# Performance work log

Measured on AMD Instinct MI355X. Metric: run time of the kernel, lower is better.

## Reference

```python
import jax, jax.numpy as jnp
import numpy as np

B, S, H = 2, 2048, 1024
NH = 16
HD = H // NH  # 64


def _linear_params(key, fan_in, fan_out):
    k1, k2 = jax.random.split(key)
    bound = 1.0 / np.sqrt(fan_in)
    W = jax.random.uniform(k1, (fan_in, fan_out), jnp.float32, -bound, bound)
    b = jax.random.uniform(k2, (fan_out,), jnp.float32, -bound, bound)
    return W, b


def setup_inputs() -> dict:
    key = jax.random.key(0)
    ks = jax.random.split(key, 7)
    hidden_states = jax.random.normal(ks[0], (B, S, H), jnp.float32)
    governance_embeddings = jax.random.normal(ks[1], (B, H), jnp.float32)
    Wq, bq = _linear_params(ks[2], H, H)
    Wk, bk = _linear_params(ks[3], H, H)
    Wv, bv = _linear_params(ks[4], H, H)
    Wgq, bgq = _linear_params(ks[5], H, H)
    Wgk, bgk = _linear_params(ks[6], H, H)
    return {
        'hidden_states': hidden_states,
        'governance_embeddings': governance_embeddings,
        'Wq': Wq, 'bq': bq, 'Wk': Wk, 'bk': bk, 'Wv': Wv, 'bv': bv,
        'Wgq': Wgq, 'bgq': bgq, 'Wgk': Wgk, 'bgk': bgk,
    }


def reference(hidden_states, governance_embeddings, Wq, bq, Wk, bk, Wv, bv, Wgq, bgq, Wgk, bgk):
    b, s, h = hidden_states.shape
    # QKV projections -> [b, nh, s, hd]
    def heads(x):
        return x.reshape(b, s, NH, HD).transpose(0, 2, 1, 3)
    q = heads(hidden_states @ Wq + bq)
    k = heads(hidden_states @ Wk + bk)
    v = heads(hidden_states @ Wv + bv)

    scale = jnp.float32(1.0 / np.sqrt(HD))
    scores = jnp.einsum('bhid,bhjd->bhij', q, k) * scale  # [b,nh,s,s]

    # governance bias: one query per example vs per-token keys (unscaled)
    gq = (governance_embeddings @ Wgq + bgq).reshape(b, NH, HD)      # [b,nh,hd]
    gk = (hidden_states @ Wgk + bgk).reshape(b, s, NH, HD)           # [b,s,nh,hd]
    gov_scores = jnp.einsum('bhd,bshd->bhs', gq, gk)                 # [b,nh,s]

    # bias is constant along key dim (torch expand on last axis)
    combined = scores + 0.1 * gov_scores[..., :, None]

    probs = jax.nn.softmax(combined, axis=-1)  # dropout = identity (eval)
    context = jnp.einsum('bhij,bhjd->bhid', probs, v)
    context = context.transpose(0, 2, 1, 3).reshape(b, s, h)

    entropy = -jnp.sum(probs * jnp.log(probs + 1e-8), axis=-1).mean()
    influence = jnp.abs(gov_scores).mean()  # mean over expanded tensor == mean over [b,nh,s]
    concentration = probs.max(axis=-1).mean()
    return context, entropy, influence, concentration
```

## Files before the change

### kernel.cpp

```cpp
#include <hip/hip_runtime.h>


typedef unsigned short u16;
typedef __attribute__((ext_vector_type(8))) short bf16x8;
typedef __attribute__((ext_vector_type(4))) float f32x4;
typedef __attribute__((ext_vector_type(16))) float f32x16;
typedef __attribute__((ext_vector_type(2))) float f32x2;
typedef __attribute__((ext_vector_type(4))) u16 u16x4;
typedef __attribute__((ext_vector_type(4))) float float4v;

typedef const __attribute__((address_space(1))) void gvoid_t;
typedef __attribute__((address_space(3))) void lvoid_t;

__device__ __forceinline__ void gl_lds16(const void* g, void* l) {
  __builtin_amdgcn_global_load_lds((gvoid_t*)g, (lvoid_t*)l, 16, 0, 0);
}

__device__ __forceinline__ u16 f2bf(float x) {
  union { float f; unsigned u; } v; v.f = x;
  unsigned r = v.u + 0x7fffu + ((v.u >> 16) & 1u);
  return (u16)(r >> 16);
}
__device__ __forceinline__ unsigned pk2(float hi, float lo) {
  union { float f; unsigned u; } a, b; a.f = hi; b.f = lo;
  return __builtin_amdgcn_perm(a.u, b.u, 0x07060302u);
}
__device__ __forceinline__ bf16x8 mk8(unsigned a, unsigned b, unsigned c, unsigned d) {
  union { unsigned u[4]; bf16x8 v; } x;
  x.u[0] = a; x.u[1] = b; x.u[2] = c; x.u[3] = d; return x.v;
}

#if defined(__has_builtin)
#if __has_builtin(__builtin_amdgcn_exp2f)
#define EXP2(x) __builtin_amdgcn_exp2f(x)
#endif
#endif
#ifndef EXP2
#define EXP2(x) exp2f(x)
#endif

__global__ void prep(const float* __restrict__ hs,
                     const float* __restrict__ W0, const float* __restrict__ W1,
                     const float* __restrict__ W2, const float* __restrict__ W3,
                     const float* __restrict__ ge, const float* __restrict__ Wgq,
                     u16* __restrict__ hsB, u16* __restrict__ WB,
                     float* __restrict__ gq_part, float* __restrict__ acc3) {
  __shared__ __align__(16) u16 T[64][72];
  int bx = blockIdx.x, tid = threadIdx.x;
  if (bx < 2048) {
    int i = bx * 256 + tid;
    const float4v* in4 = (const float4v*)hs;
    float4v a = in4[i * 2], b = in4[i * 2 + 1];
    bf16x8 v;
    v[0] = (short)f2bf(a.x); v[1] = (short)f2bf(a.y);
    v[2] = (short)f2bf(a.z); v[3] = (short)f2bf(a.w);
    v[4] = (short)f2bf(b.x); v[5] = (short)f2bf(b.y);
    v[6] = (short)f2bf(b.z); v[7] = (short)f2bf(b.w);
    *(bf16x8*)&hsB[(size_t)i * 8] = v;
    return;
  }
  if (bx < 3072) {
    int idx = bx - 2048;
    int mat = idx >> 8, sub = idx & 255;
    const float* W = (mat == 0) ? W0 : (mat == 1) ? W1 : (mat == 2) ? W2 : W3;
    int k0 = (sub >> 4) * 64, n0 = (sub & 15) * 64;
#pragma unroll
    for (int p = 0; p < 4; ++p) {
      int chunk = p * 256 + tid;
      int row = chunk >> 4, cp = chunk & 15;
      float4v v = *(const float4v*)&W[(size_t)(k0 + row) * 1024 + n0 + cp * 4];
      u16x4 o; o.x = f2bf(v.x); o.y = f2bf(v.y); o.z = f2bf(v.z); o.w = f2bf(v.w);
      *(u16x4*)&T[row][cp * 4] = o;
    }
    __syncthreads();
#pragma unroll
    for (int p = 0; p < 2; ++p) {
      int chunk = p * 256 + tid;
      int nrow = chunk >> 3, cp = chunk & 7;
      bf16x8 v;
#pragma unroll
      for (int e = 0; e < 8; ++e) v[e] = (short)T[cp * 8 + e][nrow];
      *(bf16x8*)&WB[(size_t)(mat * 1024 + n0 + nrow) * 1024 + k0 + cp * 8] = v;
    }
    return;
  }
  {
    int idx = bx - 3072;
    if (idx == 0 && tid < 3) acc3[tid] = 0.f;
    int kb = idx >> 1, b = idx & 1;
    int col0 = tid * 4;
    float4v s = {0.f, 0.f, 0.f, 0.f};
    for (int k = kb * 32; k < kb * 32 + 32; ++k) {
      float g = ge[b * 1024 + k];
      float4v w = *(const float4v*)&Wgq[(size_t)k * 1024 + col0];
      s.x += g * w.x; s.y += g * w.y; s.z += g * w.z; s.w += g * w.w;
    }
    *(float4v*)&gq_part[(size_t)idx * 1024 + col0] = s;
  }
}

__global__ __launch_bounds__(256, 3) void gemm_qkvg(
    const u16* __restrict__ A, const u16* __restrict__ Bw,
    const float* __restrict__ bq, const float* __restrict__ bk,
    const float* __restrict__ bv, const float* __restrict__ bgk,
    const float* __restrict__ bgq, const float* __restrict__ gq_part,
    u16* __restrict__ Qb, u16* __restrict__ Kt4, u16* __restrict__ Vt4,
    float* __restrict__ acc3) {
  __shared__ __align__(16) u16 As[2][128 * 32];
  __shared__ __align__(16) u16 Bs[2][128 * 32];
  __shared__ float redI[4];
  const int tid = threadIdx.x, lane = tid & 63, wv = tid >> 6;
  const int li = lane & 15, quad = lane >> 4;
  const int bid = blockIdx.x;
  const int nb = bid & 31, mb = bid >> 5;
  const u16* Ap = A + (size_t)(mb * 128) * 1024;
  const u16* Bp = Bw + (size_t)(nb * 128) * 1024;
  const int wm0 = (wv >> 1) * 64, wn0 = (wv & 1) * 64;

  f32x4 acc[4][4];
#pragma unroll
  for (int t = 0; t < 4; ++t)
#pragma unroll
    for (int u = 0; u < 4; ++u) acc[t][u] = (f32x4){0.f, 0.f, 0.f, 0.f};

#pragma unroll
  for (int jj = 0; jj < 2; ++jj) {
    int j = wv * 2 + jj;
    int row = j * 16 + (lane >> 2);
    int co = lane & 3;
    gl_lds16(Ap + (size_t)row * 1024 + co * 8, &As[0][j * 512]);
    gl_lds16(Bp + (size_t)row * 1024 + co * 8, &Bs[0][j * 512]);
  }

  for (int kt = 0; kt < 32; ++kt) {
    const int cur = kt & 1;
    __syncthreads();
    if (kt < 31) {
#pragma unroll
      for (int jj = 0; jj < 2; ++jj) {
        int j = wv * 2 + jj;
        int row = j * 16 + (lane >> 2);
        int co = lane & 3;
        gl_lds16(Ap + (size_t)row * 1024 + (kt + 1) * 32 + co * 8, &As[cur ^ 1][j * 512]);
        gl_lds16(Bp + (size_t)row * 1024 + (kt + 1) * 32 + co * 8, &Bs[cur ^ 1][j * 512]);
      }
    }
    bf16x8 af[4], bf[4];
#pragma unroll
    for (int t = 0; t < 4; ++t)
      af[t] = *(const bf16x8*)&As[cur][(wm0 + t * 16 + li) * 32 + quad * 8];
#pragma unroll
    for (int u = 0; u < 4; ++u)
      bf[u] = *(const bf16x8*)&Bs[cur][(wn0 + u * 16 + li) * 32 + quad * 8];
#pragma unroll
    for (int t = 0; t < 4; ++t)
#pragma unroll
      for (int u = 0; u < 4; ++u)
        acc[t][u] = __builtin_amdgcn_mfma_f32_16x16x32_bf16(af[t], bf[u], acc[t][u], 0, 0, 0);
  }

  const int nbase = nb * 128;
  const int mat = nbase >> 10;
  if (mat == 3) {
    const int colbase = nbase & 1023;
    const int bat = (mb * 128) >> 11;
    float gqv[4], bgkv[4];
#pragma unroll
    for (int u2 = 0; u2 < 4; ++u2) {
      int col = colbase + wn0 + u2 * 16 + li;
      float g = bgq[col];
      for (int kb = 0; kb < 32; ++kb)
        g += gq_part[(size_t)(kb * 2 + bat) * 1024 + col];
      gqv[u2] = g;
      bgkv[u2] = bgk[col];
    }
    float infl = 0.f;
#pragma unroll
    for (int t = 0; t < 4; ++t)
#pragma unroll
      for (int r = 0; r < 4; ++r) {
        float v = (acc[t][0][r] + bgkv[0]) * gqv[0];
        v = __builtin_fmaf(acc[t][1][r] + bgkv[1], gqv[1], v);
        v = __builtin_fmaf(acc[t][2][r] + bgkv[2], gqv[2], v);
        v = __builtin_fmaf(acc[t][3][r] + bgkv[3], gqv[3], v);
        v += __shfl_xor(v, 1, 64); v += __shfl_xor(v, 2, 64);
        v += __shfl_xor(v, 4, 64); v += __shfl_xor(v, 8, 64);
        infl += fabsf(v);
      }
    infl = (li == 0) ? infl : 0.f;
    infl += __shfl_xor(infl, 16, 64);
    infl += __shfl_xor(infl, 32, 64);
    if (lane == 0) redI[wv] = infl;
    __syncthreads();
    if (tid == 0) atomicAdd(&acc3[2], redI[0] + redI[1] + redI[2] + redI[3]);
  } else if (mat == 2) {
#pragma unroll
    for (int t = 0; t < 4; ++t)
#pragma unroll
      for (int u = 0; u < 4; ++u) {
        int col = (nbase & 1023) + wn0 + u * 16 + li;
        float bb = bv[col];
        int row = mb * 128 + wm0 + t * 16 + quad * 4;
        int b = row >> 11, s = row & 2047, g = s >> 2;
        uint2 w;
        w.x = pk2(acc[t][u][1] + bb, acc[t][u][0] + bb);
        w.y = pk2(acc[t][u][3] + bb, acc[t][u][2] + bb);
        *(uint2*)&Vt4[(((size_t)b * 512 + g) * 1024 + col) * 4] = w;
      }
  } else if (mat == 1) {
#pragma unroll
    for (int t = 0; t < 4; ++t)
#pragma unroll
      for (int u = 0; u < 4; ++u) {
        int col = (nbase & 1023) + wn0 + u * 16 + li;
        int h = col >> 6, g = (col & 63) >> 2, r4 = col & 3;
        float bb = bk[col];
        u16* base = &Kt4[(((size_t)(0 * 16 + h) * 16 + g) * 2048) * 4 + r4];
#pragma unroll
        for (int r = 0; r < 4; ++r) {
          int row = mb * 128 + wm0 + t * 16 + quad * 4 + r;
          int b = row >> 11, s = row & 2047;
          base[((size_t)b * 16 * 16 * 2048 + s) * 4] = f2bf(acc[t][u][r] + bb);
        }
      }
  } else {
#pragma unroll
    for (int t = 0; t < 4; ++t)
#pragma unroll
      for (int u = 0; u < 4; ++u) {
        int col = (nbase & 1023) + wn0 + u * 16 + li;
        float bb = bq[col];
#pragma unroll
        for (int r = 0; r < 4; ++r) {
          int row = mb * 128 + wm0 + t * 16 + quad * 4 + r;
          Qb[(size_t)row * 1024 + col] = f2bf((acc[t][u][r] + bb) * 0.18033688f);
        }
      }
  }
}

__global__ __launch_bounds__(256, 2) void attn_kernel(
    const u16* __restrict__ Qb, const u16* __restrict__ Kt4,
    const u16* __restrict__ Vt4, float* __restrict__ out,
    float* __restrict__ acc3 ) {
  __shared__ __align__(16) u16 Ks[2][8192];
  __shared__ __align__(16) u16 Vs[2][8192];
  __shared__ float red[8];

  const int tid = threadIdx.x, lane = tid & 63, wv = tid >> 6;
  const int q_l = lane & 31, half = lane >> 5;
  const int x8 = half << 3;
  const int bx = blockIdx.x;
  const int bh = bx & 31, qb = bx >> 5;
  const int b = bh >> 4, h = bh & 15;

  const u16* Qp = Qb + (size_t)(b * 2048 + qb * 128 + wv * 32 + q_l) * 1024 + h * 64;
  const u16* Kp4 = Kt4 + ((size_t)(b * 16 + h) * 16) * 2048 * 4;
  const u16* Vp4 = Vt4 + ((size_t)b * 512 * 1024 + h * 64) * 4;

  bf16x8 qf[4];
#pragma unroll
  for (int s = 0; s < 4; ++s)
    qf[s] = *(const bf16x8*)&Qp[s * 16 + half * 8];

  f32x2 mx2 = {-3.0e38f, -3.0e38f}, ps2 = {0.f, 0.f}, es2 = {0.f, 0.f};
  f32x16 accO[2];
#pragma unroll
  for (int dt = 0; dt < 2; ++dt)
#pragma unroll
    for (int r = 0; r < 16; ++r) accO[dt][r] = 0.f;

  const int ksrc = (2 * lane);
  const int vlane_d = 2 * (lane & 31);

#pragma unroll
  for (int jj = 0; jj < 4; ++jj) {
    int g = wv * 4 + jj;
    int xg = ((g >> 1) & 1) << 3;
    gl_lds16(Kp4 + ((size_t)g * 2048 + (ksrc ^ xg)) * 4, &Ks[0][g * 512]);
  }
#pragma unroll
  for (int jj = 0; jj < 4; ++jj) {
    int j = wv * 4 + jj;
    int g = 2 * j + (lane >> 5);
    int xg = (g & 1) << 3;
    gl_lds16(Vp4 + ((size_t)g * 1024 + (vlane_d ^ xg)) * 4, &Vs[0][j * 512]);
  }

  for (int kt = 0; kt < 16; ++kt) {
    const int cur = kt & 1;
    __syncthreads();
    if (kt < 15) {
#pragma unroll
      for (int jj = 0; jj < 4; ++jj) {
        int g = wv * 4 + jj;
        int xg = ((g >> 1) & 1) << 3;
        gl_lds16(Kp4 + ((size_t)g * 2048 + (kt + 1) * 128 + (ksrc ^ xg)) * 4,
                 &Ks[cur ^ 1][g * 512]);
      }
#pragma unroll
      for (int jj = 0; jj < 4; ++jj) {
        int j = wv * 4 + jj;
        int g = 2 * j + (lane >> 5);
        int xg = (g & 1) << 3;
        gl_lds16(Vp4 + ((size_t)((kt + 1) * 32 + g) * 1024 + (vlane_d ^ xg)) * 4,
                 &Vs[cur ^ 1][j * 512]);
      }
    }
    const u16* KsC = &Ks[cur][0];
    const u16* VsC = &Vs[cur][0];

#pragma unroll
    for (int u = 0; u < 4; ++u) {
      const int keyp = (u * 32 + q_l) ^ x8;
      f32x16 c;
#pragma unroll
      for (int r = 0; r < 16; ++r) c[r] = 0.f;
#pragma unroll
      for (int s = 0; s < 4; ++s) {
        int g0 = s * 4 + half * 2;
        uint2 k0 = *(const uint2*)&KsC[g0 * 512 + keyp * 4];
        uint2 k1 = *(const uint2*)&KsC[(g0 + 1) * 512 + keyp * 4];
        c = __builtin_amdgcn_mfma_f32_32x32x16_bf16(
            mk8(k0.x, k0.y, k1.x, k1.y), qf[s], c, 0, 0, 0);
      }
#pragma unroll
      for (int r = 0; r < 8; ++r) {
        f32x2 sv = {c[2 * r], c[2 * r + 1]};
        mx2 = __builtin_elementwise_max(mx2, sv);
        f32x2 pe = {EXP2(sv.x), EXP2(sv.y)};
        ps2 += pe;
        es2 += pe * sv;
        c[2 * r] = pe.x; c[2 * r + 1] = pe.y;
      }
      bf16x8 bf0 = mk8(pk2(c[1], c[0]),   pk2(c[3], c[2]),
                       pk2(c[5], c[4]),   pk2(c[7], c[6]));
      bf16x8 bf1 = mk8(pk2(c[9], c[8]),   pk2(c[11], c[10]),
                       pk2(c[13], c[12]), pk2(c[15], c[14]));
#pragma unroll
      for (int dt = 0; dt < 2; ++dt) {
        int dp = (dt * 32 + q_l) ^ x8;
        uint2 v0 = *(const uint2*)&VsC[(u * 8 + half) * 256 + dp * 4];
        uint2 v1 = *(const uint2*)&VsC[(u * 8 + 2 + half) * 256 + dp * 4];
        accO[dt] = __builtin_amdgcn_mfma_f32_32x32x16_bf16(
            mk8(v0.x, v0.y, v1.x, v1.y), bf0, accO[dt], 0, 0, 0);
        uint2 v2 = *(const uint2*)&VsC[(u * 8 + 4 + half) * 256 + dp * 4];
        uint2 v3 = *(const uint2*)&VsC[(u * 8 + 6 + half) * 256 + dp * 4];
        accO[dt] = __builtin_amdgcn_mfma_f32_32x32x16_bf16(
            mk8(v2.x, v2.y, v3.x, v3.y), bf1, accO[dt], 0, 0, 0);
      }
    }
  }

  float l_st = ps2.x + ps2.y, e_st = es2.x + es2.y, m_st = fmaxf(mx2.x, mx2.y);
  float lsum = l_st + __shfl_xor(l_st, 32, 64);
  float esum = e_st + __shfl_xor(e_st, 32, 64);
  float mm = fmaxf(m_st, __shfl_xor(m_st, 32, 64));
  float inv = 1.0f / lsum;
  float entw = __logf(lsum) - 0.69314718f * esum * inv;
  float concw = EXP2(mm) * inv;

  float* outp = out + (size_t)(b * 2048 + qb * 128 + wv * 32 + q_l) * 1024 + h * 64;
#pragma unroll
  for (int dt = 0; dt < 2; ++dt)
#pragma unroll
    for (int g = 0; g < 4; ++g) {
      float4v o;
      o.x = accO[dt][4 * g + 0] * inv; o.y = accO[dt][4 * g + 1] * inv;
      o.z = accO[dt][4 * g + 2] * inv; o.w = accO[dt][4 * g + 3] * inv;
      *(float4v*)&outp[dt * 32 + 8 * g + 4 * half] = o;
    }

#pragma unroll
  for (int off = 1; off < 64; off <<= 1) {
    entw += __shfl_xor(entw, off, 64);
    concw += __shfl_xor(concw, off, 64);
  }
  if (lane == 0) { red[wv] = entw * 0.5f; red[4 + wv] = concw * 0.5f; }
  __syncthreads();
  if (tid == 0) {
    atomicAdd(&acc3[0], red[0] + red[1] + red[2] + red[3]);
    atomicAdd(&acc3[1], red[4] + red[5] + red[6] + red[7]);
  }
}

__global__ void finalize(const float* __restrict__ acc3, float* __restrict__ out) {
  if (threadIdx.x == 0) {
    out[0] = acc3[0] * (1.f / 65536.f);
    out[1] = acc3[2] * (1.f / 65536.f);
    out[2] = acc3[1] * (1.f / 65536.f);
  }
}

extern "C" void kernel_launch(void* const* d_in, const int* in_sizes, int n_in,
                              void* d_out, int out_size, void* d_ws, size_t ws_size,
                              hipStream_t stream) {
  (void)in_sizes; (void)n_in; (void)out_size; (void)ws_size;
  const float* hs  = (const float*)d_in[0];
  const float* ge  = (const float*)d_in[1];
  const float* Wq  = (const float*)d_in[2];
  const float* bq  = (const float*)d_in[3];
  const float* Wk  = (const float*)d_in[4];
  const float* bk  = (const float*)d_in[5];
  const float* Wv  = (const float*)d_in[6];
  const float* bv  = (const float*)d_in[7];
  const float* Wgq = (const float*)d_in[8];
  const float* bgq = (const float*)d_in[9];
  const float* Wgk = (const float*)d_in[10];
  const float* bgk = (const float*)d_in[11];

  char* ws = (char*)d_ws;
  u16* hsB  = (u16*)(ws);
  u16* WB   = (u16*)(ws + (size_t)(8 << 20));
  u16* Qb   = (u16*)(ws + (size_t)(16 << 20));
  u16* Kt4  = (u16*)(ws + (size_t)(24 << 20));
  u16* Vt4  = (u16*)(ws + (size_t)(32 << 20));
  float* gq_part = (float*)(ws + (size_t)(48 << 20));
  float* acc3    = (float*)(ws + (size_t)(48 << 20) + 524288);
  float* out = (float*)d_out;

  prep<<<3136, 256, 0, stream>>>(hs, Wq, Wk, Wv, Wgk, ge, Wgq, hsB, WB, gq_part, acc3);
  gemm_qkvg<<<1024, 256, 0, stream>>>(hsB, WB, bq, bk, bv, bgk, bgq, gq_part,
                                      Qb, Kt4, Vt4, acc3);
  attn_kernel<<<512, 256, 0, stream>>>(Qb, Kt4, Vt4, out, acc3);
  finalize<<<1, 64, 0, stream>>>(acc3, out + 4194304);
}
```

Before: 208.0 us.

## Fuse hidden-state bf16 conversion into GEMM loads and batch attention score MFMAs

Drops the separate fp32-to-bf16 pass over hidden_states in the prep kernel. The GEMM now streams fp32 A tiles straight into XOR-swizzled LDS and truncates them to bf16 while building MFMA fragments. This removes a full write and re-read of the activation buffer, but doubles A-tile LDS traffic and footprint. It also truncates instead of rounding to nearest. Separately, the attention loop computes all four score MFMA blocks before doing exp and the PV MFMAs, which gives more independent work per phase at the cost of higher register pressure.

```diff
diff --git a/kernel.cpp b/kernel.cpp
--- a/kernel.cpp
+++ b/kernel.cpp
@@ -8,6 +8,7 @@
 typedef __attribute__((ext_vector_type(2))) float f32x2;
 typedef __attribute__((ext_vector_type(4))) u16 u16x4;
 typedef __attribute__((ext_vector_type(4))) float float4v;
+typedef __attribute__((ext_vector_type(4))) unsigned uint4v;
 
 typedef const __attribute__((address_space(1))) void gvoid_t;
 typedef __attribute__((address_space(3))) void lvoid_t;
@@ -24,6 +25,9 @@
 __device__ __forceinline__ unsigned pk2(float hi, float lo) {
   union { float f; unsigned u; } a, b; a.f = hi; b.f = lo;
   return __builtin_amdgcn_perm(a.u, b.u, 0x07060302u);
+}
+__device__ __forceinline__ unsigned pk2u(unsigned hi, unsigned lo) {
+  return __builtin_amdgcn_perm(hi, lo, 0x07060302u);
 }
 __device__ __forceinline__ bf16x8 mk8(unsigned a, unsigned b, unsigned c, unsigned d) {
   union { unsigned u[4]; bf16x8 v; } x;
@@ -39,29 +43,15 @@
 #define EXP2(x) exp2f(x)
 #endif
 
-__global__ void prep(const float* __restrict__ hs,
-                     const float* __restrict__ W0, const float* __restrict__ W1,
+__global__ void prep(const float* __restrict__ W0, const float* __restrict__ W1,
                      const float* __restrict__ W2, const float* __restrict__ W3,
                      const float* __restrict__ ge, const float* __restrict__ Wgq,
-                     u16* __restrict__ hsB, u16* __restrict__ WB,
-                     float* __restrict__ gq_part, float* __restrict__ acc3) {
+                     u16* __restrict__ WB, float* __restrict__ gq_part,
+                     float* __restrict__ acc3) {
   __shared__ __align__(16) u16 T[64][72];
   int bx = blockIdx.x, tid = threadIdx.x;
-  if (bx < 2048) {
-    int i = bx * 256 + tid;
-    const float4v* in4 = (const float4v*)hs;
-    float4v a = in4[i * 2], b = in4[i * 2 + 1];
-    bf16x8 v;
-    v[0] = (short)f2bf(a.x); v[1] = (short)f2bf(a.y);
-    v[2] = (short)f2bf(a.z); v[3] = (short)f2bf(a.w);
-    v[4] = (short)f2bf(b.x); v[5] = (short)f2bf(b.y);
-    v[6] = (short)f2bf(b.z); v[7] = (short)f2bf(b.w);
-    *(bf16x8*)&hsB[(size_t)i * 8] = v;
-    return;
-  }
-  if (bx < 3072) {
-    int idx = bx - 2048;
-    int mat = idx >> 8, sub = idx & 255;
+  if (bx < 1024) {
+    int mat = bx >> 8, sub = bx & 255;
     const float* W = (mat == 0) ? W0 : (mat == 1) ? W1 : (mat == 2) ? W2 : W3;
     int k0 = (sub >> 4) * 64, n0 = (sub & 15) * 64;
 #pragma unroll
@@ -85,7 +75,7 @@
     return;
   }
   {
-    int idx = bx - 3072;
+    int idx = bx - 1024;
     if (idx == 0 && tid < 3) acc3[tid] = 0.f;
     int kb = idx >> 1, b = idx & 1;
     int col0 = tid * 4;
@@ -100,36 +90,43 @@
 }
 
 __global__ __launch_bounds__(256, 3) void gemm_qkvg(
-    const u16* __restrict__ A, const u16* __restrict__ Bw,
+    const float* __restrict__ A, const u16* __restrict__ Bw,
     const float* __restrict__ bq, const float* __restrict__ bk,
     const float* __restrict__ bv, const float* __restrict__ bgk,
     const float* __restrict__ bgq, const float* __restrict__ gq_part,
     u16* __restrict__ Qb, u16* __restrict__ Kt4, u16* __restrict__ Vt4,
     float* __restrict__ acc3) {
-  __shared__ __align__(16) u16 As[2][128 * 32];
+  __shared__ __align__(16) float As[2][4096];
   __shared__ __align__(16) u16 Bs[2][128 * 32];
   __shared__ float redI[4];
   const int tid = threadIdx.x, lane = tid & 63, wv = tid >> 6;
   const int li = lane & 15, quad = lane >> 4;
   const int bid = blockIdx.x;
   const int nb = bid & 31, mb = bid >> 5;
-  const u16* Ap = A + (size_t)(mb * 128) * 1024;
+  const float* Ap = A + (size_t)(mb * 128) * 1024;
   const u16* Bp = Bw + (size_t)(nb * 128) * 1024;
   const int wm0 = (wv >> 1) * 64, wn0 = (wv & 1) * 64;
 
+  const int arow = (lane >> 3);
+  const int agsrc = (lane & 7) ^ arow;
+  const int brow = (lane >> 2);
+  const int bco = lane & 3;
+
   f32x4 acc[4][4];
 #pragma unroll
   for (int t = 0; t < 4; ++t)
 #pragma unroll
     for (int u = 0; u < 4; ++u) acc[t][u] = (f32x4){0.f, 0.f, 0.f, 0.f};
 
+#pragma unroll
+  for (int jj = 0; jj < 4; ++jj) {
+    int j = wv * 4 + jj;
+    gl_lds16(Ap + (size_t)(j * 8 + arow) * 1024 + agsrc * 4, &As[0][j * 256]);
+  }
 #pragma unroll
   for (int jj = 0; jj < 2; ++jj) {
     int j = wv * 2 + jj;
-    int row = j * 16 + (lane >> 2);
-    int co = lane & 3;
-    gl_lds16(Ap + (size_t)row * 1024 + co * 8, &As[0][j * 512]);
-    gl_lds16(Bp + (size_t)row * 1024 + co * 8, &Bs[0][j * 512]);
+    gl_lds16(Bp + (size_t)(j * 16 + brow) * 1024 + bco * 8, &Bs[0][j * 512]);
   }
 
   for (int kt = 0; kt < 32; ++kt) {
@@ -137,18 +134,27 @@
     __syncthreads();
     if (kt < 31) {
 #pragma unroll
+      for (int jj = 0; jj < 4; ++jj) {
+        int j = wv * 4 + jj;
+        gl_lds16(Ap + (size_t)(j * 8 + arow) * 1024 + (kt + 1) * 32 + agsrc * 4,
+                 &As[cur ^ 1][j * 256]);
+      }
+#pragma unroll
       for (int jj = 0; jj < 2; ++jj) {
         int j = wv * 2 + jj;
-        int row = j * 16 + (lane >> 2);
-        int co = lane & 3;
-        gl_lds16(Ap + (size_t)row * 1024 + (kt + 1) * 32 + co * 8, &As[cur ^ 1][j * 512]);
-        gl_lds16(Bp + (size_t)row * 1024 + (kt + 1) * 32 + co * 8, &Bs[cur ^ 1][j * 512]);
+        gl_lds16(Bp + (size_t)(j * 16 + brow) * 1024 + (kt + 1) * 32 + bco * 8,
+                 &Bs[cur ^ 1][j * 512]);
       }
     }
     bf16x8 af[4], bf[4];
 #pragma unroll
-    for (int t = 0; t < 4; ++t)
-      af[t] = *(const bf16x8*)&As[cur][(wm0 + t * 16 + li) * 32 + quad * 8];
+    for (int t = 0; t < 4; ++t) {
+      int row = wm0 + t * 16 + li;
+      int rx = row & 7;
+      uint4v v = *(const uint4v*)&As[cur][row * 32 + ((quad * 2) ^ rx) * 4];
+      uint4v w = *(const uint4v*)&As[cur][row * 32 + ((quad * 2 + 1) ^ rx) * 4];
+      af[t] = mk8(pk2u(v.y, v.x), pk2u(v.w, v.z), pk2u(w.y, w.x), pk2u(w.w, w.z));
+    }
 #pragma unroll
     for (int u = 0; u < 4; ++u)
       bf[u] = *(const bf16x8*)&Bs[cur][(wn0 + u * 16 + li) * 32 + quad * 8];
@@ -215,7 +221,7 @@
         int col = (nbase & 1023) + wn0 + u * 16 + li;
         int h = col >> 6, g = (col & 63) >> 2, r4 = col & 3;
         float bb = bk[col];
-        u16* base = &Kt4[(((size_t)(0 * 16 + h) * 16 + g) * 2048) * 4 + r4];
+        u16* base = &Kt4[(((size_t)h * 16 + g) * 2048) * 4 + r4];
 #pragma unroll
         for (int r = 0; r < 4; ++r) {
           int row = mb * 128 + wm0 + t * 16 + quad * 4 + r;
@@ -310,33 +316,40 @@
     const u16* KsC = &Ks[cur][0];
     const u16* VsC = &Vs[cur][0];
 
+    f32x16 c[4];
 #pragma unroll
     for (int u = 0; u < 4; ++u) {
       const int keyp = (u * 32 + q_l) ^ x8;
-      f32x16 c;
-#pragma unroll
-      for (int r = 0; r < 16; ++r) c[r] = 0.f;
+      f32x16 cc;
+#pragma unroll
+      for (int r = 0; r < 16; ++r) cc[r] = 0.f;
 #pragma unroll
       for (int s = 0; s < 4; ++s) {
         int g0 = s * 4 + half * 2;
         uint2 k0 = *(const uint2*)&KsC[g0 * 512 + keyp * 4];
         uint2 k1 = *(const uint2*)&KsC[(g0 + 1) * 512 + keyp * 4];
-        c = __builtin_amdgcn_mfma_f32_32x32x16_bf16(
-            mk8(k0.x, k0.y, k1.x, k1.y), qf[s], c, 0, 0, 0);
-      }
+        cc = __builtin_amdgcn_mfma_f32_32x32x16_bf16(
+            mk8(k0.x, k0.y, k1.x, k1.y), qf[s], cc, 0, 0, 0);
+      }
+      c[u] = cc;
+    }
+#pragma unroll
+    for (int u = 0; u < 4; ++u)
 #pragma unroll
       for (int r = 0; r < 8; ++r) {
-        f32x2 sv = {c[2 * r], c[2 * r + 1]};
+        f32x2 sv = {c[u][2 * r], c[u][2 * r + 1]};
         mx2 = __builtin_elementwise_max(mx2, sv);
         f32x2 pe = {EXP2(sv.x), EXP2(sv.y)};
         ps2 += pe;
         es2 += pe * sv;
-        c[2 * r] = pe.x; c[2 * r + 1] = pe.y;
-      }
-      bf16x8 bf0 = mk8(pk2(c[1], c[0]),   pk2(c[3], c[2]),
-                       pk2(c[5], c[4]),   pk2(c[7], c[6]));
-      bf16x8 bf1 = mk8(pk2(c[9], c[8]),   pk2(c[11], c[10]),
-                       pk2(c[13], c[12]), pk2(c[15], c[14]));
+        c[u][2 * r] = pe.x; c[u][2 * r + 1] = pe.y;
+      }
+#pragma unroll
+    for (int u = 0; u < 4; ++u) {
+      bf16x8 bf0 = mk8(pk2(c[u][1], c[u][0]),   pk2(c[u][3], c[u][2]),
+                       pk2(c[u][5], c[u][4]),   pk2(c[u][7], c[u][6]));
+      bf16x8 bf1 = mk8(pk2(c[u][9], c[u][8]),   pk2(c[u][11], c[u][10]),
+                       pk2(c[u][13], c[u][12]), pk2(c[u][15], c[u][14]));
 #pragma unroll
       for (int dt = 0; dt < 2; ++dt) {
         int dp = (dt * 32 + q_l) ^ x8;
@@ -410,17 +423,16 @@
   const float* bgk = (const float*)d_in[11];
 
   char* ws = (char*)d_ws;
-  u16* hsB  = (u16*)(ws);
-  u16* WB   = (u16*)(ws + (size_t)(8 << 20));
-  u16* Qb   = (u16*)(ws + (size_t)(16 << 20));
-  u16* Kt4  = (u16*)(ws + (size_t)(24 << 20));
-  u16* Vt4  = (u16*)(ws + (size_t)(32 << 20));
-  float* gq_part = (float*)(ws + (size_t)(48 << 20));
-  float* acc3    = (float*)(ws + (size_t)(48 << 20) + 524288);
+  u16* WB   = (u16*)(ws);
+  u16* Qb   = (u16*)(ws + (size_t)(8 << 20));
+  u16* Kt4  = (u16*)(ws + (size_t)(16 << 20));
+  u16* Vt4  = (u16*)(ws + (size_t)(24 << 20));
+  float* gq_part = (float*)(ws + (size_t)(32 << 20));
+  float* acc3    = (float*)(ws + (size_t)(32 << 20) + 524288);
   float* out = (float*)d_out;
 
-  prep<<<3136, 256, 0, stream>>>(hs, Wq, Wk, Wv, Wgk, ge, Wgq, hsB, WB, gq_part, acc3);
-  gemm_qkvg<<<1024, 256, 0, stream>>>(hsB, WB, bq, bk, bv, bgk, bgq, gq_part,
+  prep<<<1088, 256, 0, stream>>>(Wq, Wk, Wv, Wgk, ge, Wgq, WB, gq_part, acc3);
+  gemm_qkvg<<<1024, 256, 0, stream>>>(hs, WB, bq, bk, bv, bgk, bgq, gq_part,
                                       Qb, Kt4, Vt4, acc3);
   attn_kernel<<<512, 256, 0, stream>>>(Qb, Kt4, Vt4, out, acc3);
   finalize<<<1, 64, 0, stream>>>(acc3, out + 4194304);
```

New measurement: 228.4 us. 9.8% more time.
